# Performance work log

Hardware: AMD Instinct MI355X
Metric: run time of the kernel (lower is better)

Reference implementation:

```python
import jax, jax.numpy as jnp
import numpy as np

BN_EPS = 1e-5

def _bn_eval(x, g, b, m, v):
    # BatchNorm1d in eval mode with running stats
    return (x - m) * (g / jnp.sqrt(v + BN_EPS)) + b

def _gcn_layer(x, adj, w, b):
    # D^-0.5 A D^-0.5 (X W) + b  (same math as diag(d^-0.5) @ adj @ diag(d^-0.5))
    deg = adj.sum(axis=1)
    dis = deg ** -0.5
    xw = x @ w
    return dis[:, None] * (adj @ (dis[:, None] * xw)) + b

def setup_inputs() -> dict:
    key = jax.random.key(0)
    ks = jax.random.split(key, 8)
    N, F, E, H, G, C = 16384, 1024, 256, 256, 128, 10
    def xavier(k, i, o):
        s = float(np.sqrt(6.0 / (i + o)))
        return jax.random.uniform(k, (i, o), jnp.float32, -s, s)
    return {
        "feature": jax.random.uniform(ks[0], (N, F), jnp.float32),
        "adj": jax.random.uniform(ks[1], (N, N), jnp.float32),
        "enc_w1": xavier(ks[2], F, 512), "enc_b1": jnp.zeros((512,), jnp.float32),
        "bn1_g": jnp.ones((512,), jnp.float32), "bn1_b": jnp.zeros((512,), jnp.float32),
        "bn1_m": jnp.zeros((512,), jnp.float32), "bn1_v": jnp.ones((512,), jnp.float32),
        "enc_w2": xavier(ks[3], 512, E), "enc_b2": jnp.zeros((E,), jnp.float32),
        "bn2_g": jnp.ones((E,), jnp.float32), "bn2_b": jnp.zeros((E,), jnp.float32),
        "bn2_m": jnp.zeros((E,), jnp.float32), "bn2_v": jnp.ones((E,), jnp.float32),
        "gcn1_w": xavier(ks[4], E, H), "gcn1_b": jnp.zeros((H,), jnp.float32),
        "gcn2_w": xavier(ks[5], H, G), "gcn2_b": jnp.zeros((G,), jnp.float32),
        "cls_w": xavier(ks[6], G, C), "cls_b": jnp.zeros((C,), jnp.float32),
    }

def reference(feature, adj, enc_w1, enc_b1, bn1_g, bn1_b, bn1_m, bn1_v,
              enc_w2, enc_b2, bn2_g, bn2_b, bn2_m, bn2_v,
              gcn1_w, gcn1_b, gcn2_w, gcn2_b, cls_w, cls_b):
    # encoder.encode (eval: dropout off, BN running stats)
    h = jax.nn.relu(_bn_eval(feature @ enc_w1 + enc_b1, bn1_g, bn1_b, bn1_m, bn1_v))
    h = jax.nn.relu(_bn_eval(h @ enc_w2 + enc_b2, bn2_g, bn2_b, bn2_m, bn2_v))
    h = jax.nn.relu(_gcn_layer(h, adj, gcn1_w, gcn1_b))
    h = jax.nn.relu(_gcn_layer(h, adj, gcn2_w, gcn2_b))
    out = jax.nn.sigmoid(h @ cls_w + cls_b)
    return jnp.clip(out, 1e-10, 1 - 1e-10)
```

## Files before the change

### kernel.cpp

```cpp
#include <hip/hip_runtime.h>
#include <stdint.h>

typedef unsigned short u16;
typedef unsigned int u32;
typedef __attribute__((ext_vector_type(4))) float f32x4;
typedef __attribute__((ext_vector_type(16))) float f32x16;
typedef __attribute__((ext_vector_type(8))) short s16x8;
typedef __attribute__((ext_vector_type(4))) short s16x4;
typedef __attribute__((ext_vector_type(2))) unsigned int u32x2;
typedef __attribute__((ext_vector_type(4))) unsigned int u32x4;
typedef __attribute__((ext_vector_type(8))) int i32x8;

__device__ __forceinline__ u16 f2bf(float x){
  unsigned u = __builtin_bit_cast(unsigned, x);
  u += 0x7fffu + ((u >> 16) & 1u);
  return (u16)(u >> 16);
}
__device__ __forceinline__ float bf2f(u16 b){
  return __builtin_bit_cast(float, (unsigned)b << 16);
}
__device__ __forceinline__ u32 pk_fp8x4(float a, float b, float c, float d){
  int w = 0;
  w = __builtin_amdgcn_cvt_pk_fp8_f32(a, b, w, false);
  w = __builtin_amdgcn_cvt_pk_fp8_f32(c, d, w, true);
  return (u32)w;
}


__device__ __forceinline__ void tcvtT_dev(const float* __restrict__ src, u16* __restrict__ dst,
                                          int K, int N, int bx, int by, char* smem){
  float (*t)[33] = (float (*)[33])smem;
  int tx = threadIdx.x & 31, ty = threadIdx.x >> 5;
  int n0 = bx * 32, k0 = by * 32;
  #pragma unroll
  for (int i = 0; i < 4; i++)
    t[ty + 8 * i][tx] = src[(size_t)(k0 + ty + 8 * i) * N + n0 + tx];
  __syncthreads();
  #pragma unroll
  for (int i = 0; i < 4; i++)
    dst[(size_t)(n0 + ty + 8 * i) * K + k0 + tx] = f2bf(t[tx][ty + 8 * i]);
}

__device__ __forceinline__ void bn_dev(const float* __restrict__ g, const float* __restrict__ b,
                                       const float* __restrict__ m, const float* __restrict__ v,
                                       const float* __restrict__ lin_b,
                                       float* __restrict__ s, float* __restrict__ bb,
                                       int n, int blk){
  int i = blk * 256 + threadIdx.x;
  if (i < n){
    float sc = g[i] * rsqrtf(v[i] + 1e-5f);
    s[i] = sc;
    bb[i] = (lin_b[i] - m[i]) * sc + b[i];
  }
}

__global__ __launch_bounds__(256) void prep0_kernel(
    const float* __restrict__ enc_w1, u16* __restrict__ w1t,
    const float* __restrict__ g, const float* __restrict__ b,
    const float* __restrict__ m, const float* __restrict__ v,
    const float* __restrict__ lin_b, float* __restrict__ s1, float* __restrict__ bb1)
{
  __shared__ char smem[32 * 33 * 4 + 64];
  if (blockIdx.x < 512)
    tcvtT_dev(enc_w1, w1t, 1024, 512, blockIdx.x & 15, blockIdx.x >> 4, smem);
  else
    bn_dev(g, b, m, v, lin_b, s1, bb1, 512, blockIdx.x - 512);
}

__global__ __launch_bounds__(256) void enc1_deg_kernel(
    const float* __restrict__ feature, const u16* __restrict__ w1t,
    u16* __restrict__ h1, const float* __restrict__ cs, const float* __restrict__ cb,
    const float* __restrict__ adj, unsigned char* __restrict__ adj8,
    float* __restrict__ dis,
    const float* __restrict__ enc_w2, u16* __restrict__ w2t,
    const float* __restrict__ gcn1_w, u16* __restrict__ g1t,
    const float* __restrict__ gcn2_w, u16* __restrict__ g2t,
    const float* __restrict__ bn2_g, const float* __restrict__ bn2_b,
    const float* __restrict__ bn2_m, const float* __restrict__ bn2_v,
    const float* __restrict__ enc_b2, float* __restrict__ s2, float* __restrict__ bb2)
{
  constexpr int BM = 128, BN = 256, BK = 64, WM = 2, WN = 2;
  constexpr int N = 512, K = 1024, NADJ = 16384;
  constexpr int WTM = BM / WM, WTN = BN / WN, FM = WTM / 16, FN = WTN / 16;
  constexpr int AIT = (BM * BK) / (256 * 4);
  constexpr int BIT = (BN * BK) / (256 * 8);

  __shared__ __align__(16) char smem[BM * BK * 2 + BN * BK * 2];

  if (blockIdx.x >= 16640){
    int p = blockIdx.x - 16640;
    if (p < 128)       tcvtT_dev(enc_w2, w2t, 512, 256, p & 7, p >> 3, smem);
    else if (p < 192){ int l = p - 128; tcvtT_dev(gcn1_w, g1t, 256, 256, l & 7, l >> 3, smem); }
    else if (p < 224){ int l = p - 192; tcvtT_dev(gcn2_w, g2t, 256, 128, l & 3, l >> 2, smem); }
    else               bn_dev(bn2_g, bn2_b, bn2_m, bn2_v, enc_b2, s2, bb2, 256, 0);
    return;
  }

  if (blockIdx.x >= 256){
    int row = blockIdx.x - 256;
    const float* rp = adj + (size_t)row * NADJ;
    unsigned char* wp = adj8 + (size_t)row * NADJ;
    float s = 0.f;
    #pragma unroll
    for (int it = 0; it < 4; ++it){
      const float* p = rp + it * 4096 + threadIdx.x * 16;
      f32x4 v[4];
      #pragma unroll
      for (int j = 0; j < 4; ++j) v[j] = *(const f32x4*)(p + 4 * j);
      u32x4 o;
      #pragma unroll
      for (int j = 0; j < 4; ++j){
        s += (v[j][0] + v[j][1]) + (v[j][2] + v[j][3]);
        o[j] = pk_fp8x4(v[j][0], v[j][1], v[j][2], v[j][3]);
      }
      *(u32x4*)(wp + it * 4096 + threadIdx.x * 16) = o;
    }
    #pragma unroll
    for (int d = 32; d > 0; d >>= 1) s += __shfl_down(s, d, 64);
    float* ps = (float*)smem;
    if ((threadIdx.x & 63) == 0) ps[threadIdx.x >> 6] = s;
    __syncthreads();
    if (threadIdx.x == 0) dis[row] = rsqrtf((ps[0] + ps[1]) + (ps[2] + ps[3]));
    return;
  }

  u16* As = (u16*)smem;
  u16* Bs = (u16*)(smem + BM * BK * 2);
  const int tid = threadIdx.x;
  const int lane = tid & 63;
  const int wid = tid >> 6;
  const int wr = wid / WN;
  const int wc = wid % WN;
  const int bm = (blockIdx.x & 127) * BM;
  const int bn = (blockIdx.x >> 7) * BN;

  f32x4 arf[AIT];
  s16x8 brb[BIT];

  auto load_tiles = [&](int k0){
    #pragma unroll
    for (int i = 0; i < AIT; i++){
      int e = (i * 256 + tid) * 4; int r = e / BK, c = e % BK;
      arf[i] = *(const f32x4*)(feature + (size_t)(bm + r) * K + k0 + c);
    }
    #pragma unroll
    for (int i = 0; i < BIT; i++){
      int e = (i * 256 + tid) * 8; int r = e / BK, c = e % BK;
      brb[i] = *(const s16x8*)(w1t + (size_t)(bn + r) * K + k0 + c);
    }
  };
  auto store_tiles = [&](){
    char* Ac = (char*)As; char* Bc = (char*)Bs;
    #pragma unroll
    for (int i = 0; i < AIT; i++){
      int e = (i * 256 + tid) * 4; int r = e / BK, c = e % BK;
      int off = ((r * BK + c) * 2) ^ ((r & 7) << 4);
      s16x4 o;
      o[0] = (short)f2bf(arf[i][0]); o[1] = (short)f2bf(arf[i][1]);
      o[2] = (short)f2bf(arf[i][2]); o[3] = (short)f2bf(arf[i][3]);
      *(s16x4*)(Ac + off) = o;
    }
    #pragma unroll
    for (int i = 0; i < BIT; i++){
      int e = (i * 256 + tid) * 8; int r = e / BK, c = e % BK;
      int off = ((r * BK + c) * 2) ^ ((r & 7) << 4);
      *(s16x8*)(Bc + off) = brb[i];
    }
  };

  f32x4 acc[FM][FN];
  #pragma unroll
  for (int m = 0; m < FM; m++)
    #pragma unroll
    for (int n = 0; n < FN; n++)
      acc[m][n] = (f32x4){0.f, 0.f, 0.f, 0.f};

  const int arow0 = wr * WTM + (lane & 15);
  const int brow0 = wc * WTN + (lane & 15);
  const int kof = (lane >> 4) * 8;

  load_tiles(0);
  for (int kt = 0; kt < K / BK; ++kt){
    __syncthreads();
    store_tiles();
    __syncthreads();
    if (kt + 1 < K / BK) load_tiles((kt + 1) * BK);
    const char* Ac = (const char*)As;
    const char* Bc = (const char*)Bs;
    #pragma unroll
    for (int ks = 0; ks < BK / 32; ++ks){
      s16x8 af[FM], bfr[FN];
      #pragma unroll
      for (int m = 0; m < FM; m++){
        int r = arow0 + m * 16;
        af[m] = *(const s16x8*)(Ac + (((r * BK + ks * 32 + kof) * 2) ^ ((r & 7) << 4)));
      }
      #pragma unroll
      for (int n = 0; n < FN; n++){
        int r = brow0 + n * 16;
        bfr[n] = *(const s16x8*)(Bc + (((r * BK + ks * 32 + kof) * 2) ^ ((r & 7) << 4)));
      }
      #pragma unroll
      for (int m = 0; m < FM; m++)
        #pragma unroll
        for (int n = 0; n < FN; n++)
          acc[m][n] = __builtin_amdgcn_mfma_f32_16x16x32_bf16(af[m], bfr[n], acc[m][n], 0, 0, 0);
    }
  }
  #pragma unroll
  for (int m = 0; m < FM; m++){
    #pragma unroll
    for (int n = 0; n < FN; n++){
      int col = bn + wc * WTN + n * 16 + (lane & 15);
      int row0 = bm + wr * WTM + m * 16 + (lane >> 4) * 4;
      #pragma unroll
      for (int r4 = 0; r4 < 4; r4++){
        float vv = fmaxf(acc[m][n][r4] * cs[col] + cb[col], 0.f);
        h1[(size_t)(row0 + r4) * N + col] = f2bf(vv);
      }
    }
  }
}

__global__ __launch_bounds__(256, 1)
void h2tT_kernel(const u16* __restrict__ h1, const u16* __restrict__ w2t,
                 const float* __restrict__ s2, const float* __restrict__ bb2,
                 const u16* __restrict__ g1t, const float* __restrict__ dis,
                 unsigned char* __restrict__ tT)
{
  constexpr int M = 16384, K1 = 512, E = 256, K2 = 256, BK = 64;
  constexpr float SC = 256.f;

  __shared__ u16 As[64 * BK];
  __shared__ u16 Bs[256 * BK];
  __shared__ u16 H2s[64 * 256];

  const int tid = threadIdx.x;
  const int lane = tid & 63;
  const int wc = tid >> 6;
  const int bm = blockIdx.x * 64;
  const int arow0 = lane & 15;
  const int kof = (lane >> 4) * 8;

  {
    s16x8 arb[2], brb[8];
    auto load1 = [&](int k0){
      #pragma unroll
      for (int i = 0; i < 2; i++){
        int e = (i * 256 + tid) * 8; int r = e >> 6, c = e & 63;
        arb[i] = *(const s16x8*)(h1 + (size_t)(bm + r) * K1 + k0 + c);
      }
      #pragma unroll
      for (int i = 0; i < 8; i++){
        int e = (i * 256 + tid) * 8; int r = e >> 6, c = e & 63;
        brb[i] = *(const s16x8*)(w2t + (size_t)r * K1 + k0 + c);
      }
    };
    auto store1 = [&](){
      char* Ac = (char*)As; char* Bc = (char*)Bs;
      #pragma unroll
      for (int i = 0; i < 2; i++){
        int e = (i * 256 + tid) * 8; int r = e >> 6, c = e & 63;
        *(s16x8*)(Ac + (((r * BK + c) * 2) ^ ((r & 7) << 4))) = arb[i];
      }
      #pragma unroll
      for (int i = 0; i < 8; i++){
        int e = (i * 256 + tid) * 8; int r = e >> 6, c = e & 63;
        *(s16x8*)(Bc + (((r * BK + c) * 2) ^ ((r & 7) << 4))) = brb[i];
      }
    };

    f32x4 acc[4][4];
    #pragma unroll
    for (int m = 0; m < 4; m++)
      #pragma unroll
      for (int n = 0; n < 4; n++)
        acc[m][n] = (f32x4){0.f, 0.f, 0.f, 0.f};

    load1(0);
    for (int kt = 0; kt < K1 / BK; ++kt){
      __syncthreads();
      store1();
      __syncthreads();
      if (kt + 1 < K1 / BK) load1((kt + 1) * BK);
      const char* Ac = (const char*)As;
      const char* Bc = (const char*)Bs;
      #pragma unroll
      for (int ks = 0; ks < 2; ++ks){
        s16x8 af[4], bfr[4];
        #pragma unroll
        for (int m = 0; m < 4; m++){
          int r = arow0 + m * 16;
          af[m] = *(const s16x8*)(Ac + (((r * BK + ks * 32 + kof) * 2) ^ ((r & 7) << 4)));
        }
        #pragma unroll
        for (int n = 0; n < 4; n++){
          int r = wc * 64 + n * 16 + (lane & 15);
          bfr[n] = *(const s16x8*)(Bc + (((r * BK + ks * 32 + kof) * 2) ^ ((r & 7) << 4)));
        }
        #pragma unroll
        for (int m = 0; m < 4; m++)
          #pragma unroll
          for (int n = 0; n < 4; n++)
            acc[m][n] = __builtin_amdgcn_mfma_f32_16x16x32_bf16(af[m], bfr[n], acc[m][n], 0, 0, 0);
      }
    }
    __syncthreads();
    char* Hc = (char*)H2s;
    #pragma unroll
    for (int m = 0; m < 4; m++){
      #pragma unroll
      for (int n = 0; n < 4; n++){
        int col = wc * 64 + n * 16 + (lane & 15);
        int row0 = m * 16 + (lane >> 4) * 4;
        #pragma unroll
        for (int r4 = 0; r4 < 4; r4++){
          int row = row0 + r4;
          float vv = fmaxf(acc[m][n][r4] * s2[col] + bb2[col], 0.f);
          *(u16*)(Hc + (((row * 256 + col) * 2) ^ ((row & 7) << 4))) = f2bf(vv);
        }
      }
    }
  }

  {
    s16x8 brb[8];
    auto load2 = [&](int k0){
      #pragma unroll
      for (int i = 0; i < 8; i++){
        int e = (i * 256 + tid) * 8; int r = e >> 6, c = e & 63;
        brb[i] = *(const s16x8*)(g1t + (size_t)r * K2 + k0 + c);
      }
    };
    auto store2 = [&](){
      char* Bc = (char*)Bs;
      #pragma unroll
      for (int i = 0; i < 8; i++){
        int e = (i * 256 + tid) * 8; int r = e >> 6, c = e & 63;
        *(s16x8*)(Bc + (((r * BK + c) * 2) ^ ((r & 7) << 4))) = brb[i];
      }
    };

    f32x4 acc[4][4];
    #pragma unroll
    for (int m = 0; m < 4; m++)
      #pragma unroll
      for (int n = 0; n < 4; n++)
        acc[m][n] = (f32x4){0.f, 0.f, 0.f, 0.f};

    load2(0);
    for (int kt = 0; kt < K2 / BK; ++kt){
      __syncthreads();
      store2();
      __syncthreads();
      if (kt + 1 < K2 / BK) load2((kt + 1) * BK);
      const char* Hc = (const char*)H2s;
      const char* Bc = (const char*)Bs;
      #pragma unroll
      for (int ks = 0; ks < 2; ++ks){
        s16x8 af[4], bfr[4];
        #pragma unroll
        for (int m = 0; m < 4; m++){
          int r = arow0 + m * 16;
          af[m] = *(const s16x8*)(Hc + (((r * 256 + kt * 64 + ks * 32 + kof) * 2) ^ ((r & 7) << 4)));
        }
        #pragma unroll
        for (int n = 0; n < 4; n++){
          int r = wc * 64 + n * 16 + (lane & 15);
          bfr[n] = *(const s16x8*)(Bc + (((r * BK + ks * 32 + kof) * 2) ^ ((r & 7) << 4)));
        }
        #pragma unroll
        for (int m = 0; m < 4; m++)
          #pragma unroll
          for (int n = 0; n < 4; n++)
            acc[m][n] = __builtin_amdgcn_mfma_f32_16x16x32_bf16(af[m], bfr[n], acc[m][n], 0, 0, 0);
      }
    }
    #pragma unroll
    for (int m = 0; m < 4; m++){
      #pragma unroll
      for (int n = 0; n < 4; n++){
        int col = wc * 64 + n * 16 + (lane & 15);
        int row0 = bm + m * 16 + (lane >> 4) * 4;
        float v0 = acc[m][n][0] * dis[row0 + 0] * SC;
        float v1 = acc[m][n][1] * dis[row0 + 1] * SC;
        float v2 = acc[m][n][2] * dis[row0 + 2] * SC;
        float v3 = acc[m][n][3] * dis[row0 + 3] * SC;
        *(u32*)(tT + (size_t)col * M + row0) = pk_fp8x4(v0, v1, v2, v3);
      }
    }
  }
}

template<int BM, int BN>
__global__ __launch_bounds__(512, 1)
void gemm_mx(const unsigned char* __restrict__ A8, const unsigned char* __restrict__ B8,
             float* __restrict__ P, int M, int N, int K, int Ksub)
{
  constexpr int BK = 128;
  constexpr int AT = BM * BK;
  constexpr int BT = BN * BK;
  constexpr int AIT = AT / (512 * 16);
  constexpr int BIT = BT / (512 * 16);
  constexpr int WM = 2, WN = 4;
  constexpr int WTM = BM / WM;
  constexpr int WTN = BN / WN;
  constexpr int FM = WTM / 32;
  constexpr int FN = WTN / 32;
  static_assert(AIT >= 1 && BIT >= 1, "staging");

  __shared__ __align__(16) char LDS[2 * (AT + BT)];

  const int tid = threadIdx.x;
  const int lane = tid & 63;
  const int wid = tid >> 6;
  const int wr = wid >> 2;
  const int wc = wid & 3;
  const int bm = blockIdx.x * BM;
  const int kz = blockIdx.z * Ksub;

  auto stage = [&](int half, int k0){
    char* ab = LDS + half * (AT + BT);
    #pragma unroll
    for (int i = 0; i < AIT; i++){
      int e = (i * 512 + tid) * 16;
      int r = e >> 7, c = e & 127;
      int cc = c ^ ((r & 7) << 4);
      const unsigned char* g = A8 + (size_t)(bm + r) * K + k0 + cc;
      __builtin_amdgcn_global_load_lds((const __attribute__((address_space(1))) unsigned int*)g,
          (__attribute__((address_space(3))) unsigned int*)(ab + e), 16, 0, 0);
    }
    char* bb = ab + AT;
    #pragma unroll
    for (int i = 0; i < BIT; i++){
      int e = (i * 512 + tid) * 16;
      int r = e >> 7, c = e & 127;
      int cc = c ^ ((r & 7) << 4);
      const unsigned char* g = B8 + (size_t)r * K + k0 + cc;
      __builtin_amdgcn_global_load_lds((const __attribute__((address_space(1))) unsigned int*)g,
          (__attribute__((address_space(3))) unsigned int*)(bb + e), 16, 0, 0);
    }
  };

  f32x16 acc[FM][FN];
  #pragma unroll
  for (int m = 0; m < FM; m++)
    #pragma unroll
    for (int n = 0; n < FN; n++)
      #pragma unroll
      for (int i = 0; i < 16; i++)
        acc[m][n][i] = 0.f;

  const int nk = Ksub / BK;
  stage(0, kz);
  for (int kt = 0; kt < nk; ++kt){
    __syncthreads();
    if (kt + 1 < nk) stage((kt + 1) & 1, kz + (kt + 1) * BK);
    const char* ab = LDS + (kt & 1) * (AT + BT);
    const char* bb = ab + AT;
    #pragma unroll
    for (int ks = 0; ks < 2; ks++){
      const int c0 = ks * 64 + (lane >> 5) * 32;
      i32x8 af[FM], bf_[FN];
      #pragma unroll
      for (int m = 0; m < FM; m++){
        int r = wr * WTM + m * 32 + (lane & 31);
        int sw = (r & 7) << 4;
        int o = r * BK + c0;
        u32x4 lo = *(const u32x4*)(ab + (o ^ sw));
        u32x4 hi = *(const u32x4*)(ab + ((o + 16) ^ sw));
        af[m][0] = lo[0]; af[m][1] = lo[1]; af[m][2] = lo[2]; af[m][3] = lo[3];
        af[m][4] = hi[0]; af[m][5] = hi[1]; af[m][6] = hi[2]; af[m][7] = hi[3];
      }
      #pragma unroll
      for (int n = 0; n < FN; n++){
        int r = wc * WTN + n * 32 + (lane & 31);
        int sw = (r & 7) << 4;
        int o = r * BK + c0;
        u32x4 lo = *(const u32x4*)(bb + (o ^ sw));
        u32x4 hi = *(const u32x4*)(bb + ((o + 16) ^ sw));
        bf_[n][0] = lo[0]; bf_[n][1] = lo[1]; bf_[n][2] = lo[2]; bf_[n][3] = lo[3];
        bf_[n][4] = hi[0]; bf_[n][5] = hi[1]; bf_[n][6] = hi[2]; bf_[n][7] = hi[3];
      }
      #pragma unroll
      for (int m = 0; m < FM; m++)
        #pragma unroll
        for (int n = 0; n < FN; n++)
          acc[m][n] = __builtin_amdgcn_mfma_scale_f32_32x32x64_f8f6f4(
              af[m], bf_[n], acc[m][n], 0, 0, 0, 0x7F7F7F7F, 0, 0x7F7F7F7F);
    }
  }

  float* Pz = P + (size_t)blockIdx.z * M * N;
  #pragma unroll
  for (int m = 0; m < FM; m++){
    #pragma unroll
    for (int n = 0; n < FN; n++){
      int colg = wc * WTN + n * 32 + (lane & 31);
      int rbase = bm + wr * WTM + m * 32 + (lane >> 5) * 4;
      #pragma unroll
      for (int i = 0; i < 16; i++){
        int rowg = rbase + (i & 3) + 8 * (i >> 2);
        Pz[(size_t)rowg * N + colg] = acc[m][n][i];
      }
    }
  }
}

__global__ __launch_bounds__(256, 1)
void t2g_kernel(const float* __restrict__ part, const float* __restrict__ dis,
                const float* __restrict__ g1b, const u16* __restrict__ g2t,
                unsigned char* __restrict__ t2T)
{
  constexpr int M = 16384, H = 256, BK = 64;
  constexpr float SC = 256.f, SCI = 1.f / 256.f;
  const size_t MN = (size_t)M * H;

  __shared__ u16 As[64 * BK];
  __shared__ u16 Bs[128 * BK];

  const int tid = threadIdx.x;
  const int lane = tid & 63;
  const int wid = tid >> 6;
  const int wr = wid >> 1;
  const int wc = wid & 1;
  const int bm = blockIdx.x * 64;
  const int kof = (lane >> 4) * 8;

  f32x4 a0r[4], a1r[4], gbr[4];
  float dsr[4];
  s16x8 brb[4];

  auto load_tiles = [&](int k0){
    #pragma unroll
    for (int i = 0; i < 4; i++){
      int e = (i * 256 + tid) * 4; int r = e >> 6, c = e & 63;
      size_t pi = (size_t)(bm + r) * H + k0 + c;
      a0r[i] = *(const f32x4*)(part + pi);
      a1r[i] = *(const f32x4*)(part + MN + pi);
      gbr[i] = *(const f32x4*)(g1b + k0 + c);
      dsr[i] = dis[bm + r];
    }
    #pragma unroll
    for (int i = 0; i < 4; i++){
      int e = (i * 256 + tid) * 8; int r = e >> 6, c = e & 63;
      brb[i] = *(const s16x8*)(g2t + (size_t)r * H + k0 + c);
    }
  };
  auto store_tiles = [&](){
    char* Ac = (char*)As; char* Bc = (char*)Bs;
    #pragma unroll
    for (int i = 0; i < 4; i++){
      int e = (i * 256 + tid) * 4; int r = e >> 6, c = e & 63;
      float dsc = dsr[i] * SCI;
      s16x4 o;
      #pragma unroll
      for (int j = 0; j < 4; j++){
        float vv = fmaxf(dsc * (a0r[i][j] + a1r[i][j]) + gbr[i][j], 0.f);
        o[j] = (short)f2bf(vv);
      }
      *(s16x4*)(Ac + (((r * BK + c) * 2) ^ ((r & 7) << 4))) = o;
    }
    #pragma unroll
    for (int i = 0; i < 4; i++){
      int e = (i * 256 + tid) * 8; int r = e >> 6, c = e & 63;
      *(s16x8*)(Bc + (((r * BK + c) * 2) ^ ((r & 7) << 4))) = brb[i];
    }
  };

  f32x4 acc[2][4];
  #pragma unroll
  for (int m = 0; m < 2; m++)
    #pragma unroll
    for (int n = 0; n < 4; n++)
      acc[m][n] = (f32x4){0.f, 0.f, 0.f, 0.f};

  load_tiles(0);
  for (int kt = 0; kt < H / BK; ++kt){
    __syncthreads();
    store_tiles();
    __syncthreads();
    if (kt + 1 < H / BK) load_tiles((kt + 1) * BK);
    const char* Ac = (const char*)As;
    const char* Bc = (const char*)Bs;
    #pragma unroll
    for (int ks = 0; ks < 2; ++ks){
      s16x8 af[2], bfr[4];
      #pragma unroll
      for (int m = 0; m < 2; m++){
        int r = wr * 32 + m * 16 + (lane & 15);
        af[m] = *(const s16x8*)(Ac + (((r * BK + ks * 32 + kof) * 2) ^ ((r & 7) << 4)));
      }
      #pragma unroll
      for (int n = 0; n < 4; n++){
        int r = wc * 64 + n * 16 + (lane & 15);
        bfr[n] = *(const s16x8*)(Bc + (((r * BK + ks * 32 + kof) * 2) ^ ((r & 7) << 4)));
      }
      #pragma unroll
      for (int m = 0; m < 2; m++)
        #pragma unroll
        for (int n = 0; n < 4; n++)
          acc[m][n] = __builtin_amdgcn_mfma_f32_16x16x32_bf16(af[m], bfr[n], acc[m][n], 0, 0, 0);
    }
  }

  #pragma unroll
  for (int m = 0; m < 2; m++){
    #pragma unroll
    for (int n = 0; n < 4; n++){
      int col = wc * 64 + n * 16 + (lane & 15);
      int row0 = bm + wr * 32 + m * 16 + (lane >> 4) * 4;
      float v0 = acc[m][n][0] * dis[row0 + 0] * SC;
      float v1 = acc[m][n][1] * dis[row0 + 1] * SC;
      float v2 = acc[m][n][2] * dis[row0 + 2] * SC;
      float v3 = acc[m][n][3] * dis[row0 + 3] * SC;
      *(u32*)(t2T + (size_t)col * M + row0) = pk_fp8x4(v0, v1, v2, v3);
    }
  }
}

__global__ __launch_bounds__(256) void cls2_kernel(const float* __restrict__ part,
                                                   const float* __restrict__ dis,
                                                   const float* __restrict__ g2b,
                                                   const float* __restrict__ w,
                                                   const float* __restrict__ b,
                                                   float* __restrict__ out)
{
  constexpr int M = 16384, G = 128;
  constexpr float SCI = 1.f / 256.f;
  const size_t MN = (size_t)M * G;
  __shared__ float ws_[G * 10];
  __shared__ float bs_[10];
  __shared__ float gb_[G];
  for (int i = threadIdx.x; i < G * 10; i += 256) ws_[i] = w[i];
  if (threadIdx.x < 10) bs_[threadIdx.x] = b[threadIdx.x];
  if (threadIdx.x < G) gb_[threadIdx.x] = g2b[threadIdx.x];
  __syncthreads();
  int row = blockIdx.x * 256 + threadIdx.x;
  const float* p0 = part + (size_t)row * G;
  const float* p1 = p0 + MN;
  float dr = dis[row] * SCI;
  float acc[10];
  #pragma unroll
  for (int c = 0; c < 10; c++) acc[c] = bs_[c];
  for (int k16 = 0; k16 < G; k16 += 16){
    f32x4 a0[4], a1[4];
    #pragma unroll
    for (int j = 0; j < 4; j++){
      a0[j] = *(const f32x4*)(p0 + k16 + 4 * j);
      a1[j] = *(const f32x4*)(p1 + k16 + 4 * j);
    }
    #pragma unroll
    for (int j = 0; j < 16; j++){
      float h = fmaxf(dr * (a0[j >> 2][j & 3] + a1[j >> 2][j & 3]) + gb_[k16 + j], 0.f);
      #pragma unroll
      for (int c = 0; c < 10; c++) acc[c] = fmaf(h, ws_[(k16 + j) * 10 + c], acc[c]);
    }
  }
  #pragma unroll
  for (int c = 0; c < 10; c++){
    float sg = 1.f / (1.f + expf(-acc[c]));
    sg = fminf(fmaxf(sg, 1e-10f), 1.f - 1e-10f);
    out[(size_t)row * 10 + c] = sg;
  }
}


extern "C" void kernel_launch(void* const* d_in, const int* in_sizes, int n_in,
                              void* d_out, int out_size, void* d_ws, size_t ws_size,
                              hipStream_t stream)
{
  (void)in_sizes; (void)n_in; (void)out_size; (void)ws_size;
  const float* feature = (const float*)d_in[0];
  const float* adj     = (const float*)d_in[1];
  const float* enc_w1  = (const float*)d_in[2];
  const float* enc_b1  = (const float*)d_in[3];
  const float* bn1_g   = (const float*)d_in[4];
  const float* bn1_b   = (const float*)d_in[5];
  const float* bn1_m   = (const float*)d_in[6];
  const float* bn1_v   = (const float*)d_in[7];
  const float* enc_w2  = (const float*)d_in[8];
  const float* enc_b2  = (const float*)d_in[9];
  const float* bn2_g   = (const float*)d_in[10];
  const float* bn2_b   = (const float*)d_in[11];
  const float* bn2_m   = (const float*)d_in[12];
  const float* bn2_v   = (const float*)d_in[13];
  const float* gcn1_w  = (const float*)d_in[14];
  const float* gcn1_b  = (const float*)d_in[15];
  const float* gcn2_w  = (const float*)d_in[16];
  const float* gcn2_b  = (const float*)d_in[17];
  const float* cls_w   = (const float*)d_in[18];
  const float* cls_b   = (const float*)d_in[19];
  float* out = (float*)d_out;

  const int NN = 16384, F = 1024, H1 = 512, E = 256, H = 256, G = 128;

  char* ws = (char*)d_ws;
  size_t off = 0;
  auto alloc = [&](size_t bytes) -> char* {
    char* p = ws + off; off += (bytes + 255) & ~(size_t)255; return p;
  };
  float* dis = (float*)alloc((size_t)NN * 4);
  float* s1  = (float*)alloc((size_t)H1 * 4);
  float* bb1 = (float*)alloc((size_t)H1 * 4);
  float* s2  = (float*)alloc((size_t)E * 4);
  float* bb2 = (float*)alloc((size_t)E * 4);
  u16* w1t = (u16*)alloc((size_t)H1 * F * 2);
  u16* w2t = (u16*)alloc((size_t)E * H1 * 2);
  u16* g1t = (u16*)alloc((size_t)H * E * 2);
  u16* g2t = (u16*)alloc((size_t)G * H * 2);
  u16* h1  = (u16*)alloc((size_t)NN * H1 * 2);
  unsigned char* tT  = (unsigned char*)alloc((size_t)E * NN);
  unsigned char* t2T = (unsigned char*)alloc((size_t)G * NN);
  float* part = (float*)alloc((size_t)2 * NN * H * 4);
  unsigned char* adj8 = (unsigned char*)alloc((size_t)NN * NN);

  prep0_kernel<<<514, 256, 0, stream>>>(enc_w1, w1t, bn1_g, bn1_b, bn1_m, bn1_v, enc_b1, s1, bb1);

  enc1_deg_kernel<<<256 + NN + 225, 256, 0, stream>>>(
      feature, w1t, h1, s1, bb1, adj, adj8, dis,
      enc_w2, w2t, gcn1_w, g1t, gcn2_w, g2t,
      bn2_g, bn2_b, bn2_m, bn2_v, enc_b2, s2, bb2);

  h2tT_kernel<<<NN / 64, 256, 0, stream>>>(h1, w2t, s2, bb2, g1t, dis, tT);

  gemm_mx<128,256><<<dim3(NN/128, 1, 2), 512, 0, stream>>>(
      adj8, tT, part, NN, H, NN, NN/2);

  t2g_kernel<<<NN / 64, 256, 0, stream>>>(part, dis, gcn1_b, g2t, t2T);

  gemm_mx<128,128><<<dim3(NN/128, 1, 2), 512, 0, stream>>>(
      adj8, t2T, part, NN, G, NN, NN/2);

  cls2_kernel<<<NN / 256, 256, 0, stream>>>(part, dis, gcn2_b, cls_w, cls_b, out);
}
```

Before: 494.9 us.

## Fuse GCN epilogues into full-K FP8 adjacency GEMMs, drop split-K partials

The split-K gemm_mx plus separate t2g/cls2 kernels are replaced by two full-K FP8 MX GEMM kernels with 64-row tiles. Each kernel applies its epilogue in place: the GCN1 bias/relu and the second-layer weight GEMM, then the GCN2 bias/relu and the classifier with sigmoid. This removes the fp32 partial-sum buffer writes and reads and two kernel launches. h2tT is also retiled to 512 threads across 8 waves. In exchange each block runs the full 16K K loop, and the smaller tiles lower data reuse per block.

Result: slower. 527.5 us (+6.6%).

```diff
diff --git a/kernel.cpp b/kernel.cpp
--- a/kernel.cpp
+++ b/kernel.cpp
@@ -222,13 +222,13 @@
   }
 }
 
-__global__ __launch_bounds__(256, 1)
+__global__ __launch_bounds__(512, 2)
 void h2tT_kernel(const u16* __restrict__ h1, const u16* __restrict__ w2t,
                  const float* __restrict__ s2, const float* __restrict__ bb2,
                  const u16* __restrict__ g1t, const float* __restrict__ dis,
                  unsigned char* __restrict__ tT)
 {
-  constexpr int M = 16384, K1 = 512, E = 256, K2 = 256, BK = 64;
+  constexpr int M = 16384, K1 = 512, K2 = 256, BK = 64;
   constexpr float SC = 256.f;
 
   __shared__ u16 As[64 * BK];
@@ -237,42 +237,37 @@
 
   const int tid = threadIdx.x;
   const int lane = tid & 63;
-  const int wc = tid >> 6;
+  const int wid = tid >> 6;
+  const int wr = wid >> 2;
+  const int wc = wid & 3;
   const int bm = blockIdx.x * 64;
-  const int arow0 = lane & 15;
   const int kof = (lane >> 4) * 8;
 
   {
-    s16x8 arb[2], brb[8];
+    s16x8 arb, brb[4];
     auto load1 = [&](int k0){
-      #pragma unroll
-      for (int i = 0; i < 2; i++){
-        int e = (i * 256 + tid) * 8; int r = e >> 6, c = e & 63;
-        arb[i] = *(const s16x8*)(h1 + (size_t)(bm + r) * K1 + k0 + c);
-      }
-      #pragma unroll
-      for (int i = 0; i < 8; i++){
-        int e = (i * 256 + tid) * 8; int r = e >> 6, c = e & 63;
+      { int e = tid * 8; int r = e >> 6, c = e & 63;
+        arb = *(const s16x8*)(h1 + (size_t)(bm + r) * K1 + k0 + c); }
+      #pragma unroll
+      for (int i = 0; i < 4; i++){
+        int e = (i * 512 + tid) * 8; int r = e >> 6, c = e & 63;
         brb[i] = *(const s16x8*)(w2t + (size_t)r * K1 + k0 + c);
       }
     };
     auto store1 = [&](){
       char* Ac = (char*)As; char* Bc = (char*)Bs;
-      #pragma unroll
-      for (int i = 0; i < 2; i++){
-        int e = (i * 256 + tid) * 8; int r = e >> 6, c = e & 63;
-        *(s16x8*)(Ac + (((r * BK + c) * 2) ^ ((r & 7) << 4))) = arb[i];
-      }
-      #pragma unroll
-      for (int i = 0; i < 8; i++){
-        int e = (i * 256 + tid) * 8; int r = e >> 6, c = e & 63;
+      { int e = tid * 8; int r = e >> 6, c = e & 63;
+        *(s16x8*)(Ac + (((r * BK + c) * 2) ^ ((r & 7) << 4))) = arb; }
+      #pragma unroll
+      for (int i = 0; i < 4; i++){
+        int e = (i * 512 + tid) * 8; int r = e >> 6, c = e & 63;
         *(s16x8*)(Bc + (((r * BK + c) * 2) ^ ((r & 7) << 4))) = brb[i];
       }
     };
 
-    f32x4 acc[4][4];
-    #pragma unroll
-    for (int m = 0; m < 4; m++)
+    f32x4 acc[2][4];
+    #pragma unroll
+    for (int m = 0; m < 2; m++)
       #pragma unroll
       for (int n = 0; n < 4; n++)
         acc[m][n] = (f32x4){0.f, 0.f, 0.f, 0.f};
@@ -287,10 +282,10 @@
       const char* Bc = (const char*)Bs;
       #pragma unroll
       for (int ks = 0; ks < 2; ++ks){
-        s16x8 af[4], bfr[4];
-        #pragma unroll
-        for (int m = 0; m < 4; m++){
-          int r = arow0 + m * 16;
+        s16x8 af[2], bfr[4];
+        #pragma unroll
+        for (int m = 0; m < 2; m++){
+          int r = wr * 32 + m * 16 + (lane & 15);
           af[m] = *(const s16x8*)(Ac + (((r * BK + ks * 32 + kof) * 2) ^ ((r & 7) << 4)));
         }
         #pragma unroll
@@ -299,7 +294,7 @@
           bfr[n] = *(const s16x8*)(Bc + (((r * BK + ks * 32 + kof) * 2) ^ ((r & 7) << 4)));
         }
         #pragma unroll
-        for (int m = 0; m < 4; m++)
+        for (int m = 0; m < 2; m++)
           #pragma unroll
           for (int n = 0; n < 4; n++)
             acc[m][n] = __builtin_amdgcn_mfma_f32_16x16x32_bf16(af[m], bfr[n], acc[m][n], 0, 0, 0);
@@ -308,11 +303,11 @@
     __syncthreads();
     char* Hc = (char*)H2s;
     #pragma unroll
-    for (int m = 0; m < 4; m++){
+    for (int m = 0; m < 2; m++){
       #pragma unroll
       for (int n = 0; n < 4; n++){
         int col = wc * 64 + n * 16 + (lane & 15);
-        int row0 = m * 16 + (lane >> 4) * 4;
+        int row0 = wr * 32 + m * 16 + (lane >> 4) * 4;
         #pragma unroll
         for (int r4 = 0; r4 < 4; r4++){
           int row = row0 + r4;
@@ -324,26 +319,26 @@
   }
 
   {
-    s16x8 brb[8];
+    s16x8 brb[4];
     auto load2 = [&](int k0){
       #pragma unroll
-      for (int i = 0; i < 8; i++){
-        int e = (i * 256 + tid) * 8; int r = e >> 6, c = e & 63;
+      for (int i = 0; i < 4; i++){
+        int e = (i * 512 + tid) * 8; int r = e >> 6, c = e & 63;
         brb[i] = *(const s16x8*)(g1t + (size_t)r * K2 + k0 + c);
       }
     };
     auto store2 = [&](){
       char* Bc = (char*)Bs;
       #pragma unroll
-      for (int i = 0; i < 8; i++){
-        int e = (i * 256 + tid) * 8; int r = e >> 6, c = e & 63;
+      for (int i = 0; i < 4; i++){
+        int e = (i * 512 + tid) * 8; int r = e >> 6, c = e & 63;
         *(s16x8*)(Bc + (((r * BK + c) * 2) ^ ((r & 7) << 4))) = brb[i];
       }
     };
 
-    f32x4 acc[4][4];
-    #pragma unroll
-    for (int m = 0; m < 4; m++)
+    f32x4 acc[2][4];
+    #pragma unroll
+    for (int m = 0; m < 2; m++)
       #pragma unroll
       for (int n = 0; n < 4; n++)
         acc[m][n] = (f32x4){0.f, 0.f, 0.f, 0.f};
@@ -358,10 +353,10 @@
       const char* Bc = (const char*)Bs;
       #pragma unroll
       for (int ks = 0; ks < 2; ++ks){
-        s16x8 af[4], bfr[4];
-        #pragma unroll
-        for (int m = 0; m < 4; m++){
-          int r = arow0 + m * 16;
+        s16x8 af[2], bfr[4];
+        #pragma unroll
+        for (int m = 0; m < 2; m++){
+          int r = wr * 32 + m * 16 + (lane & 15);
           af[m] = *(const s16x8*)(Hc + (((r * 256 + kt * 64 + ks * 32 + kof) * 2) ^ ((r & 7) << 4)));
         }
         #pragma unroll
@@ -370,18 +365,18 @@
           bfr[n] = *(const s16x8*)(Bc + (((r * BK + ks * 32 + kof) * 2) ^ ((r & 7) << 4)));
         }
         #pragma unroll
-        for (int m = 0; m < 4; m++)
+        for (int m = 0; m < 2; m++)
           #pragma unroll
           for (int n = 0; n < 4; n++)
             acc[m][n] = __builtin_amdgcn_mfma_f32_16x16x32_bf16(af[m], bfr[n], acc[m][n], 0, 0, 0);
       }
     }
     #pragma unroll
-    for (int m = 0; m < 4; m++){
+    for (int m = 0; m < 2; m++){
       #pragma unroll
       for (int n = 0; n < 4; n++){
         int col = wc * 64 + n * 16 + (lane & 15);
-        int row0 = bm + m * 16 + (lane >> 4) * 4;
+        int row0 = bm + wr * 32 + m * 16 + (lane >> 4) * 4;
         float v0 = acc[m][n][0] * dis[row0 + 0] * SC;
         float v1 = acc[m][n][1] * dis[row0 + 1] * SC;
         float v2 = acc[m][n][2] * dis[row0 + 2] * SC;
@@ -392,22 +387,15 @@
   }
 }
 
-template<int BM, int BN>
-__global__ __launch_bounds__(512, 1)
-void gemm_mx(const unsigned char* __restrict__ A8, const unsigned char* __restrict__ B8,
-             float* __restrict__ P, int M, int N, int K, int Ksub)
+__global__ __launch_bounds__(512, 4)
+void mx1t2_kernel(const unsigned char* __restrict__ A8, const unsigned char* __restrict__ B8,
+                  const float* __restrict__ dis, const float* __restrict__ g1b,
+                  const u16* __restrict__ g2t, unsigned char* __restrict__ t2T)
 {
-  constexpr int BK = 128;
+  constexpr int M = 16384, K = 16384, BK = 128, BM = 64;
   constexpr int AT = BM * BK;
-  constexpr int BT = BN * BK;
-  constexpr int AIT = AT / (512 * 16);
-  constexpr int BIT = BT / (512 * 16);
-  constexpr int WM = 2, WN = 4;
-  constexpr int WTM = BM / WM;
-  constexpr int WTN = BN / WN;
-  constexpr int FM = WTM / 32;
-  constexpr int FN = WTN / 32;
-  static_assert(AIT >= 1 && BIT >= 1, "staging");
+  constexpr int BT = 256 * BK;
+  constexpr float SC = 256.f, SCI = 1.f / 256.f;
 
   __shared__ __align__(16) char LDS[2 * (AT + BT)];
 
@@ -417,22 +405,18 @@
   const int wr = wid >> 2;
   const int wc = wid & 3;
   const int bm = blockIdx.x * BM;
-  const int kz = blockIdx.z * Ksub;
 
   auto stage = [&](int half, int k0){
     char* ab = LDS + half * (AT + BT);
-    #pragma unroll
-    for (int i = 0; i < AIT; i++){
-      int e = (i * 512 + tid) * 16;
+    { int e = tid * 16;
       int r = e >> 7, c = e & 127;
       int cc = c ^ ((r & 7) << 4);
       const unsigned char* g = A8 + (size_t)(bm + r) * K + k0 + cc;
       __builtin_amdgcn_global_load_lds((const __attribute__((address_space(1))) unsigned int*)g,
-          (__attribute__((address_space(3))) unsigned int*)(ab + e), 16, 0, 0);
-    }
+          (__attribute__((address_space(3))) unsigned int*)(ab + e), 16, 0, 0); }
     char* bb = ab + AT;
     #pragma unroll
-    for (int i = 0; i < BIT; i++){
+    for (int i = 0; i < 4; i++){
       int e = (i * 512 + tid) * 16;
       int r = e >> 7, c = e & 127;
       int cc = c ^ ((r & 7) << 4);
@@ -442,226 +426,236 @@
     }
   };
 
-  f32x16 acc[FM][FN];
+  f32x16 acc[2];
   #pragma unroll
-  for (int m = 0; m < FM; m++)
-    #pragma unroll
-    for (int n = 0; n < FN; n++)
-      #pragma unroll
-      for (int i = 0; i < 16; i++)
-        acc[m][n][i] = 0.f;
-
-  const int nk = Ksub / BK;
-  stage(0, kz);
-  for (int kt = 0; kt < nk; ++kt){
+  for (int n = 0; n < 2; n++)
+    #pragma unroll
+    for (int i = 0; i < 16; i++) acc[n][i] = 0.f;
+
+  stage(0, 0);
+  for (int kt = 0; kt < K / BK; ++kt){
     __syncthreads();
-    if (kt + 1 < nk) stage((kt + 1) & 1, kz + (kt + 1) * BK);
+    if (kt + 1 < K / BK) stage((kt + 1) & 1, (kt + 1) * BK);
     const char* ab = LDS + (kt & 1) * (AT + BT);
     const char* bb = ab + AT;
     #pragma unroll
     for (int ks = 0; ks < 2; ks++){
       const int c0 = ks * 64 + (lane >> 5) * 32;
-      i32x8 af[FM], bf_[FN];
-      #pragma unroll
-      for (int m = 0; m < FM; m++){
-        int r = wr * WTM + m * 32 + (lane & 31);
+      i32x8 af, bf_[2];
+      { int r = wr * 32 + (lane & 31);
         int sw = (r & 7) << 4;
         int o = r * BK + c0;
         u32x4 lo = *(const u32x4*)(ab + (o ^ sw));
         u32x4 hi = *(const u32x4*)(ab + ((o + 16) ^ sw));
-        af[m][0] = lo[0]; af[m][1] = lo[1]; af[m][2] = lo[2]; af[m][3] = lo[3];
-        af[m][4] = hi[0]; af[m][5] = hi[1]; af[m][6] = hi[2]; af[m][7] = hi[3];
-      }
-      #pragma unroll
-      for (int n = 0; n < FN; n++){
-        int r = wc * WTN + n * 32 + (lane & 31);
+        af[0]=lo[0];af[1]=lo[1];af[2]=lo[2];af[3]=lo[3];
+        af[4]=hi[0];af[5]=hi[1];af[6]=hi[2];af[7]=hi[3]; }
+      #pragma unroll
+      for (int n = 0; n < 2; n++){
+        int r = wc * 64 + n * 32 + (lane & 31);
         int sw = (r & 7) << 4;
         int o = r * BK + c0;
         u32x4 lo = *(const u32x4*)(bb + (o ^ sw));
         u32x4 hi = *(const u32x4*)(bb + ((o + 16) ^ sw));
-        bf_[n][0] = lo[0]; bf_[n][1] = lo[1]; bf_[n][2] = lo[2]; bf_[n][3] = lo[3];
-        bf_[n][4] = hi[0]; bf_[n][5] = hi[1]; bf_[n][6] = hi[2]; bf_[n][7] = hi[3];
-      }
-      #pragma unroll
-      for (int m = 0; m < FM; m++)
-        #pragma unroll
-        for (int n = 0; n < FN; n++)
-          acc[m][n] = __builtin_amdgcn_mfma_scale_f32_32x32x64_f8f6f4(
-              af[m], bf_[n], acc[m][n], 0, 0, 0, 0x7F7F7F7F, 0, 0x7F7F7F7F);
-    }
-  }
-
-  float* Pz = P + (size_t)blockIdx.z * M * N;
+        bf_[n][0]=lo[0];bf_[n][1]=lo[1];bf_[n][2]=lo[2];bf_[n][3]=lo[3];
+        bf_[n][4]=hi[0];bf_[n][5]=hi[1];bf_[n][6]=hi[2];bf_[n][7]=hi[3];
+      }
+      #pragma unroll
+      for (int n = 0; n < 2; n++)
+        acc[n] = __builtin_amdgcn_mfma_scale_f32_32x32x64_f8f6f4(
+            af, bf_[n], acc[n], 0, 0, 0, 0x7F7F7F7F, 0, 0x7F7F7F7F);
+    }
+  }
+
+  __syncthreads();
+  u16* H3 = (u16*)LDS;
+  u16* B2 = (u16*)(LDS + 32768);
+  {
+    int colg0 = wc * 64 + (lane & 31);
+    int rb = wr * 32 + (lane >> 5) * 4;
+    float gb0 = g1b[colg0], gb1 = g1b[colg0 + 32];
+    #pragma unroll
+    for (int i = 0; i < 16; i++){
+      int row = rb + (i & 3) + 8 * (i >> 2);
+      float dr = dis[bm + row] * SCI;
+      float v0 = fmaxf(dr * acc[0][i] + gb0, 0.f);
+      float v1 = fmaxf(dr * acc[1][i] + gb1, 0.f);
+      *(u16*)((char*)H3 + (((row * 256 + colg0) * 2) ^ ((row & 7) << 4))) = f2bf(v0);
+      *(u16*)((char*)H3 + (((row * 256 + colg0 + 32) * 2) ^ ((row & 7) << 4))) = f2bf(v1);
+    }
+  }
+
+  f32x4 acc2[2][2];
   #pragma unroll
-  for (int m = 0; m < FM; m++){
-    #pragma unroll
-    for (int n = 0; n < FN; n++){
-      int colg = wc * WTN + n * 32 + (lane & 31);
-      int rbase = bm + wr * WTM + m * 32 + (lane >> 5) * 4;
-      #pragma unroll
-      for (int i = 0; i < 16; i++){
-        int rowg = rbase + (i & 3) + 8 * (i >> 2);
-        Pz[(size_t)rowg * N + colg] = acc[m][n][i];
-      }
-    }
-  }
-}
-
-__global__ __launch_bounds__(256, 1)
-void t2g_kernel(const float* __restrict__ part, const float* __restrict__ dis,
-                const float* __restrict__ g1b, const u16* __restrict__ g2t,
-                unsigned char* __restrict__ t2T)
+  for (int m = 0; m < 2; m++)
+    #pragma unroll
+    for (int n = 0; n < 2; n++)
+      acc2[m][n] = (f32x4){0.f, 0.f, 0.f, 0.f};
+  const int kof = (lane >> 4) * 8;
+
+  for (int kt2 = 0; kt2 < 4; ++kt2){
+    s16x8 br[2];
+    #pragma unroll
+    for (int i = 0; i < 2; i++){
+      int e = (i * 512 + tid) * 8; int r = e >> 6, c = e & 63;
+      br[i] = *(const s16x8*)(g2t + (size_t)r * 256 + kt2 * 64 + c);
+    }
+    __syncthreads();
+    #pragma unroll
+    for (int i = 0; i < 2; i++){
+      int e = (i * 512 + tid) * 8; int r = e >> 6, c = e & 63;
+      *(s16x8*)((char*)B2 + (((r * 64 + c) * 2) ^ ((r & 7) << 4))) = br[i];
+    }
+    __syncthreads();
+    #pragma unroll
+    for (int ks = 0; ks < 2; ++ks){
+      s16x8 af[2], bf[2];
+      #pragma unroll
+      for (int m = 0; m < 2; m++){
+        int r = wr * 32 + m * 16 + (lane & 15);
+        af[m] = *(const s16x8*)((const char*)H3 + (((r * 256 + kt2 * 64 + ks * 32 + kof) * 2) ^ ((r & 7) << 4)));
+      }
+      #pragma unroll
+      for (int n = 0; n < 2; n++){
+        int r = wc * 32 + n * 16 + (lane & 15);
+        bf[n] = *(const s16x8*)((const char*)B2 + (((r * 64 + ks * 32 + kof) * 2) ^ ((r & 7) << 4)));
+      }
+      #pragma unroll
+      for (int m = 0; m < 2; m++)
+        #pragma unroll
+        for (int n = 0; n < 2; n++)
+          acc2[m][n] = __builtin_amdgcn_mfma_f32_16x16x32_bf16(af[m], bf[n], acc2[m][n], 0, 0, 0);
+    }
+  }
+
+  #pragma unroll
+  for (int m = 0; m < 2; m++){
+    #pragma unroll
+    for (int n = 0; n < 2; n++){
+      int col = wc * 32 + n * 16 + (lane & 15);
+      int row0 = bm + wr * 32 + m * 16 + (lane >> 4) * 4;
+      float v0 = acc2[m][n][0] * dis[row0 + 0] * SC;
+      float v1 = acc2[m][n][1] * dis[row0 + 1] * SC;
+      float v2 = acc2[m][n][2] * dis[row0 + 2] * SC;
+      float v3 = acc2[m][n][3] * dis[row0 + 3] * SC;
+      *(u32*)(t2T + (size_t)col * M + row0) = pk_fp8x4(v0, v1, v2, v3);
+    }
+  }
+}
+
+__global__ __launch_bounds__(512, 4)
+void mx2cls_kernel(const unsigned char* __restrict__ A8, const unsigned char* __restrict__ B8,
+                   const float* __restrict__ dis, const float* __restrict__ g2b,
+                   const float* __restrict__ cls_w, const float* __restrict__ cls_b,
+                   float* __restrict__ out)
 {
-  constexpr int M = 16384, H = 256, BK = 64;
-  constexpr float SC = 256.f, SCI = 1.f / 256.f;
-  const size_t MN = (size_t)M * H;
-
-  __shared__ u16 As[64 * BK];
-  __shared__ u16 Bs[128 * BK];
+  constexpr int M = 16384, K = 16384, BK = 128, BM = 64;
+  constexpr int AT = BM * BK;
+  constexpr int BT = 128 * BK;
+  constexpr float SCI = 1.f / 256.f;
+
+  __shared__ __align__(16) char LDS[2 * (AT + BT)];
 
   const int tid = threadIdx.x;
   const int lane = tid & 63;
   const int wid = tid >> 6;
-  const int wr = wid >> 1;
-  const int wc = wid & 1;
-  const int bm = blockIdx.x * 64;
-  const int kof = (lane >> 4) * 8;
-
-  f32x4 a0r[4], a1r[4], gbr[4];
-  float dsr[4];
-  s16x8 brb[4];
-
-  auto load_tiles = [&](int k0){
-    #pragma unroll
-    for (int i = 0; i < 4; i++){
-      int e = (i * 256 + tid) * 4; int r = e >> 6, c = e & 63;
-      size_t pi = (size_t)(bm + r) * H + k0 + c;
-      a0r[i] = *(const f32x4*)(part + pi);
-      a1r[i] = *(const f32x4*)(part + MN + pi);
-      gbr[i] = *(const f32x4*)(g1b + k0 + c);
-      dsr[i] = dis[bm + r];
-    }
-    #pragma unroll
-    for (int i = 0; i < 4; i++){
-      int e = (i * 256 + tid) * 8; int r = e >> 6, c = e & 63;
-      brb[i] = *(const s16x8*)(g2t + (size_t)r * H + k0 + c);
+  const int wr = wid >> 2;
+  const int wc = wid & 3;
+  const int bm = blockIdx.x * BM;
+
+  auto stage = [&](int half, int k0){
+    char* ab = LDS + half * (AT + BT);
+    { int e = tid * 16;
+      int r = e >> 7, c = e & 127;
+      int cc = c ^ ((r & 7) << 4);
+      const unsigned char* g = A8 + (size_t)(bm + r) * K + k0 + cc;
+      __builtin_amdgcn_global_load_lds((const __attribute__((address_space(1))) unsigned int*)g,
+          (__attribute__((address_space(3))) unsigned int*)(ab + e), 16, 0, 0); }
+    char* bb = ab + AT;
+    #pragma unroll
+    for (int i = 0; i < 2; i++){
+      int e = (i * 512 + tid) * 16;
+      int r = e >> 7, c = e & 127;
+      int cc = c ^ ((r & 7) << 4);
+      const unsigned char* g = B8 + (size_t)r * K + k0 + cc;
+      __builtin_amdgcn_global_load_lds((const __attribute__((address_space(1))) unsigned int*)g,
+          (__attribute__((address_space(3))) unsigned int*)(bb + e), 16, 0, 0);
     }
   };
-  auto store_tiles = [&](){
-    char* Ac = (char*)As; char* Bc = (char*)Bs;
-    #pragma unroll
-    for (int i = 0; i < 4; i++){
-      int e = (i * 256 + tid) * 4; int r = e >> 6, c = e & 63;
-      float dsc = dsr[i] * SCI;
-      s16x4 o;
-      #pragma unroll
-      for (int j = 0; j < 4; j++){
-        float vv = fmaxf(dsc * (a0r[i][j] + a1r[i][j]) + gbr[i][j], 0.f);
-        o[j] = (short)f2bf(vv);
-      }
-      *(s16x4*)(Ac + (((r * BK + c) * 2) ^ ((r & 7) << 4))) = o;
-    }
-    #pragma unroll
-    for (int i = 0; i < 4; i++){
-      int e = (i * 256 + tid) * 8; int r = e >> 6, c = e & 63;
-      *(s16x8*)(Bc + (((r * BK + c) * 2) ^ ((r & 7) << 4))) = brb[i];
-    }
-  };
-
-  f32x4 acc[2][4];
+
+  f32x16 acc;
   #pragma unroll
-  for (int m = 0; m < 2; m++)
-    #pragma unroll
-    for (int n = 0; n < 4; n++)
-      acc[m][n] = (f32x4){0.f, 0.f, 0.f, 0.f};
-
-  load_tiles(0);
-  for (int kt = 0; kt < H / BK; ++kt){
+  for (int i = 0; i < 16; i++) acc[i] = 0.f;
+
+  stage(0, 0);
+  for (int kt = 0; kt < K / BK; ++kt){
     __syncthreads();
-    store_tiles();
-    __syncthreads();
-    if (kt + 1 < H / BK) load_tiles((kt + 1) * BK);
-    const char* Ac = (const char*)As;
-    const char* Bc = (const char*)Bs;
-    #pragma unroll
-    for (int ks = 0; ks < 2; ++ks){
-      s16x8 af[2], bfr[4];
-      #pragma unroll
-      for (int m = 0; m < 2; m++){
-        int r = wr * 32 + m * 16 + (lane & 15);
-        af[m] = *(const s16x8*)(Ac + (((r * BK + ks * 32 + kof) * 2) ^ ((r & 7) << 4)));
-      }
-      #pragma unroll
-      for (int n = 0; n < 4; n++){
-        int r = wc * 64 + n * 16 + (lane & 15);
-        bfr[n] = *(const s16x8*)(Bc + (((r * BK + ks * 32 + kof) * 2) ^ ((r & 7) << 4)));
-      }
-      #pragma unroll
-      for (int m = 0; m < 2; m++)
-        #pragma unroll
-        for (int n = 0; n < 4; n++)
-          acc[m][n] = __builtin_amdgcn_mfma_f32_16x16x32_bf16(af[m], bfr[n], acc[m][n], 0, 0, 0);
-    }
-  }
-
-  #pragma unroll
-  for (int m = 0; m < 2; m++){
-    #pragma unroll
-    for (int n = 0; n < 4; n++){
-      int col = wc * 64 + n * 16 + (lane & 15);
-      int row0 = bm + wr * 32 + m * 16 + (lane >> 4) * 4;
-      float v0 = acc[m][n][0] * dis[row0 + 0] * SC;
-      float v1 = acc[m][n][1] * dis[row0 + 1] * SC;
-      float v2 = acc[m][n][2] * dis[row0 + 2] * SC;
-      float v3 = acc[m][n][3] * dis[row0 + 3] * SC;
-      *(u32*)(t2T + (size_t)col * M + row0) = pk_fp8x4(v0, v1, v2, v3);
-    }
-  }
-}
-
-__global__ __launch_bounds__(256) void cls2_kernel(const float* __restrict__ part,
-                                                   const float* __restrict__ dis,
-                                                   const float* __restrict__ g2b,
-                                                   const float* __restrict__ w,
-                                                   const float* __restrict__ b,
-                                                   float* __restrict__ out)
-{
-  constexpr int M = 16384, G = 128;
-  constexpr float SCI = 1.f / 256.f;
-  const size_t MN = (size_t)M * G;
-  __shared__ float ws_[G * 10];
-  __shared__ float bs_[10];
-  __shared__ float gb_[G];
-  for (int i = threadIdx.x; i < G * 10; i += 256) ws_[i] = w[i];
-  if (threadIdx.x < 10) bs_[threadIdx.x] = b[threadIdx.x];
-  if (threadIdx.x < G) gb_[threadIdx.x] = g2b[threadIdx.x];
+    if (kt + 1 < K / BK) stage((kt + 1) & 1, (kt + 1) * BK);
+    const char* ab = LDS + (kt & 1) * (AT + BT);
+    const char* bb = ab + AT;
+    #pragma unroll
+    for (int ks = 0; ks < 2; ks++){
+      const int c0 = ks * 64 + (lane >> 5) * 32;
+      i32x8 af, bf_;
+      { int r = wr * 32 + (lane & 31);
+        int sw = (r & 7) << 4;
+        int o = r * BK + c0;
+        u32x4 lo = *(const u32x4*)(ab + (o ^ sw));
+        u32x4 hi = *(const u32x4*)(ab + ((o + 16) ^ sw));
+        af[0]=lo[0];af[1]=lo[1];af[2]=lo[2];af[3]=lo[3];
+        af[4]=hi[0];af[5]=hi[1];af[6]=hi[2];af[7]=hi[3]; }
+      { int r = wc * 32 + (lane & 31);
+        int sw = (r & 7) << 4;
+        int o = r * BK + c0;
+        u32x4 lo = *(const u32x4*)(bb + (o ^ sw));
+        u32x4 hi = *(const u32x4*)(bb + ((o + 16) ^ sw));
+        bf_[0]=lo[0];bf_[1]=lo[1];bf_[2]=lo[2];bf_[3]=lo[3];
+        bf_[4]=hi[0];bf_[5]=hi[1];bf_[6]=hi[2];bf_[7]=hi[3]; }
+      acc = __builtin_amdgcn_mfma_scale_f32_32x32x64_f8f6f4(
+          af, bf_, acc, 0, 0, 0, 0x7F7F7F7F, 0, 0x7F7F7F7F);
+    }
+  }
+
   __syncthreads();
-  int row = blockIdx.x * 256 + threadIdx.x;
-  const float* p0 = part + (size_t)row * G;
-  const float* p1 = p0 + MN;
-  float dr = dis[row] * SCI;
-  float acc[10];
-  #pragma unroll
-  for (int c = 0; c < 10; c++) acc[c] = bs_[c];
-  for (int k16 = 0; k16 < G; k16 += 16){
-    f32x4 a0[4], a1[4];
-    #pragma unroll
-    for (int j = 0; j < 4; j++){
-      a0[j] = *(const f32x4*)(p0 + k16 + 4 * j);
-      a1[j] = *(const f32x4*)(p1 + k16 + 4 * j);
-    }
-    #pragma unroll
-    for (int j = 0; j < 16; j++){
-      float h = fmaxf(dr * (a0[j >> 2][j & 3] + a1[j >> 2][j & 3]) + gb_[k16 + j], 0.f);
-      #pragma unroll
-      for (int c = 0; c < 10; c++) acc[c] = fmaf(h, ws_[(k16 + j) * 10 + c], acc[c]);
-    }
-  }
-  #pragma unroll
-  for (int c = 0; c < 10; c++){
-    float sg = 1.f / (1.f + expf(-acc[c]));
-    sg = fminf(fmaxf(sg, 1e-10f), 1.f - 1e-10f);
-    out[(size_t)row * 10 + c] = sg;
+  float* H4  = (float*)LDS;
+  float* wsm = (float*)(LDS + 33280);
+  float* bsm = (float*)(LDS + 38400);
+  {
+    int colg = wc * 32 + (lane & 31);
+    int rb = wr * 32 + (lane >> 5) * 4;
+    float gb = g2b[colg];
+    #pragma unroll
+    for (int i = 0; i < 16; i++){
+      int row = rb + (i & 3) + 8 * (i >> 2);
+      float vv = fmaxf(dis[bm + row] * SCI * acc[i] + gb, 0.f);
+      H4[row * 130 + colg] = vv;
+    }
+  }
+  for (int i = tid; i < 1280; i += 512) wsm[i] = cls_w[i];
+  if (tid < 10) bsm[tid] = cls_b[tid];
+  __syncthreads();
+
+  if (tid < 128){
+    int row = tid >> 1, half = tid & 1;
+    float a[10];
+    #pragma unroll
+    for (int c = 0; c < 10; c++) a[c] = 0.f;
+    const float* hp = H4 + row * 130 + half * 64;
+    const float* wp0 = wsm + half * 64 * 10;
+    for (int k = 0; k < 64; ++k){
+      float h = hp[k];
+      #pragma unroll
+      for (int c = 0; c < 10; c++) a[c] = fmaf(h, wp0[k * 10 + c], a[c]);
+    }
+    #pragma unroll
+    for (int c = 0; c < 10; c++) a[c] += __shfl_xor(a[c], 1);
+    if (half == 0){
+      #pragma unroll
+      for (int c = 0; c < 10; c++){
+        float sg = 1.f / (1.f + expf(-(a[c] + bsm[c])));
+        sg = fminf(fmaxf(sg, 1e-10f), 1.f - 1e-10f);
+        out[(size_t)(bm + row) * 10 + c] = sg;
+      }
+    }
   }
 }
 
@@ -712,7 +706,6 @@
   u16* h1  = (u16*)alloc((size_t)NN * H1 * 2);
   unsigned char* tT  = (unsigned char*)alloc((size_t)E * NN);
   unsigned char* t2T = (unsigned char*)alloc((size_t)G * NN);
-  float* part = (float*)alloc((size_t)2 * NN * H * 4);
   unsigned char* adj8 = (unsigned char*)alloc((size_t)NN * NN);
 
   prep0_kernel<<<514, 256, 0, stream>>>(enc_w1, w1t, bn1_g, bn1_b, bn1_m, bn1_v, enc_b1, s1, bb1);
@@ -722,15 +715,9 @@
       enc_w2, w2t, gcn1_w, g1t, gcn2_w, g2t,
       bn2_g, bn2_b, bn2_m, bn2_v, enc_b2, s2, bb2);
 
-  h2tT_kernel<<<NN / 64, 256, 0, stream>>>(h1, w2t, s2, bb2, g1t, dis, tT);
-
-  gemm_mx<128,256><<<dim3(NN/128, 1, 2), 512, 0, stream>>>(
-      adj8, tT, part, NN, H, NN, NN/2);
-
-  t2g_kernel<<<NN / 64, 256, 0, stream>>>(part, dis, gcn1_b, g2t, t2T);
-
-  gemm_mx<128,128><<<dim3(NN/128, 1, 2), 512, 0, stream>>>(
-      adj8, t2T, part, NN, G, NN, NN/2);
-
-  cls2_kernel<<<NN / 256, 256, 0, stream>>>(part, dis, gcn2_b, cls_w, cls_b, out);
-}
+  h2tT_kernel<<<NN / 64, 512, 0, stream>>>(h1, w2t, s2, bb2, g1t, dis, tT);
+
+  mx1t2_kernel<<<NN / 64, 512, 0, stream>>>(adj8, tT, dis, gcn1_b, g2t, t2T);
+
+  mx2cls_kernel<<<NN / 64, 512, 0, stream>>>(adj8, t2T, dis, gcn2_b, cls_w, cls_b, out);
+}
```
